# Kernel optimization log

Measured on AMD Instinct MI355X. Metric: run time of the kernel, lower is better.

Reference implementation:

```python
import jax, jax.numpy as jnp
import numpy as np

HEADS = 16
KV_HEADS = 4
HEAD_DIM = 64
EMBED = 1024


def setup_inputs() -> dict:
    key = jax.random.key(0)
    k1, k2, k3, k4, k5 = jax.random.split(key, 5)
    B, S, G, E = 1, 2048, 2, EMBED
    scale = 1.0 / np.sqrt(E)
    x = jax.random.normal(k1, (B, S, G, E), dtype=jnp.float32)
    Wq = jax.random.normal(k2, (E, HEADS * HEAD_DIM), dtype=jnp.float32) * scale
    Wk = jax.random.normal(k3, (E, KV_HEADS * HEAD_DIM), dtype=jnp.float32) * scale
    Wv = jax.random.normal(k4, (E, KV_HEADS * HEAD_DIM), dtype=jnp.float32) * scale
    Wo = jax.random.normal(k5, (E, E), dtype=jnp.float32) * scale
    return {"x": x, "Wq": Wq, "Wk": Wk, "Wv": Wv, "Wo": Wo}


def reference(x, Wq, Wk, Wv, Wo):
    B, S, G, E = x.shape
    ratio = HEADS // KV_HEADS
    # projections over last dim (no bias, no activation)
    q = (x @ Wq).reshape(B, S, G, HEADS, HEAD_DIM)
    k = (x @ Wk).reshape(B, S, G, KV_HEADS, HEAD_DIM)
    v = (x @ Wv).reshape(B, S, G, KV_HEADS, HEAD_DIM)
    # GQA repeat_kv: each kv head repeated `ratio` times consecutively
    k = jnp.repeat(k, ratio, axis=3)  # [B,S,G,H,D]
    v = jnp.repeat(v, ratio, axis=3)
    # energy: [B,G,H,Q,K]
    energy = jnp.einsum('bqghd,bkghd->bghqk', q, k)
    # causal mask: triu(1) set to -inf (before the sqrt scaling, as in source)
    causal = jnp.triu(jnp.ones((S, S), dtype=bool), 1)
    energy = jnp.where(causal, -jnp.inf, energy)
    scores = jax.nn.softmax(energy / np.sqrt(HEAD_DIM), axis=-1)
    attn = jnp.einsum('bghqv,bvghd->bqghd', scores, v)
    attn = attn.reshape(B, S, G, E)
    return attn @ Wo
```

## Files before the change

kernel.cpp:

```cpp
#include <hip/hip_runtime.h>
#include <cstdint>
#include <cstddef>

typedef __bf16 bf16_t;
typedef bf16_t bf16x8 __attribute__((ext_vector_type(8)));
typedef float f32x4 __attribute__((ext_vector_type(4)));

__device__ inline bf16x8 load8(const float* p) {
  f32x4 a = *reinterpret_cast<const f32x4*>(p);
  f32x4 b = *reinterpret_cast<const f32x4*>(p + 4);
  bf16x8 r;
  r[0] = (bf16_t)a[0]; r[1] = (bf16_t)a[1];
  r[2] = (bf16_t)a[2]; r[3] = (bf16_t)a[3];
  r[4] = (bf16_t)b[0]; r[5] = (bf16_t)b[1];
  r[6] = (bf16_t)b[2]; r[7] = (bf16_t)b[3];
  return r;
}
__device__ inline bf16x8 load8(const bf16_t* p) {
  return *reinterpret_cast<const bf16x8*>(p);
}

__device__ inline void gload_lds16(const bf16_t* g, bf16_t* l) {
  __builtin_amdgcn_global_load_lds(
      (const __attribute__((address_space(1))) void*)g,
      (__attribute__((address_space(3))) void*)l, 16, 0, 0);
}

__global__ __launch_bounds__(256) void cvt_all_k(
    const float* __restrict__ x, bf16_t* __restrict__ xb,
    const float* __restrict__ Wq, const float* __restrict__ Wk,
    const float* __restrict__ Wv, const float* __restrict__ Wo,
    bf16_t* __restrict__ wqT, bf16_t* __restrict__ wkT,
    bf16_t* __restrict__ wvT, bf16_t* __restrict__ woT) {
  __shared__ bf16_t Ts[64][72];
  const int tid = threadIdx.x;
  if (blockIdx.x < 2048) {
    const size_t i = (size_t)blockIdx.x * 2048 + (size_t)tid * 8;
    *reinterpret_cast<bf16x8*>(xb + i) = load8(x + i);
    return;
  }
  const int b = blockIdx.x - 2048;
  const float* S;
  bf16_t* D;
  int N, idx;
  if (b < 256) { S = Wq; D = wqT; N = 1024; idx = b; }
  else if (b < 320) { S = Wk; D = wkT; N = 256; idx = b - 256; }
  else if (b < 384) { S = Wv; D = wvT; N = 256; idx = b - 320; }
  else { S = Wo; D = woT; N = 1024; idx = b - 384; }
  const int ntl = (N == 1024) ? 4 : 2;
  const int kt0 = (idx >> ntl) * 64;
  const int n0 = (idx & ((1 << ntl) - 1)) * 64;
#pragma unroll
  for (int i = 0; i < 2; ++i) {
    const int c = tid + 256 * i;
    const int row = c >> 3, col0 = (c & 7) * 8;
    *reinterpret_cast<bf16x8*>(&Ts[row][col0]) =
        load8(&S[(size_t)(kt0 + row) * N + n0 + col0]);
  }
  __syncthreads();
#pragma unroll
  for (int i = 0; i < 2; ++i) {
    const int c = tid + 256 * i;
    const int nrow = c >> 3, k0 = (c & 7) * 8;
    bf16x8 v;
#pragma unroll
    for (int j = 0; j < 8; ++j) v[j] = Ts[k0 + j][nrow];
    *reinterpret_cast<bf16x8*>(&D[(size_t)(n0 + nrow) * 1024 + kt0 + k0]) = v;
  }
}

__device__ inline void stage_gldsA(const bf16_t* __restrict__ G, int grow0,
                                   int gK, int k0, bf16_t* lds, int w, int l) {
#pragma unroll
  for (int i = 0; i < 2; ++i) {
    const int seg = w * 2 + i;
    const int r = (seg << 4) + (l >> 2);
    const int cb = (l & 3) ^ ((r >> 1) & 3);
    gload_lds16(G + (size_t)(grow0 + r) * gK + k0 + cb * 8, lds + (seg << 9));
  }
}
__device__ inline void stage_gldsB(const bf16_t* __restrict__ G, int grow0,
                                   int gK, int k0, bf16_t* lds, int w, int l) {
  const int r = (w << 4) + (l >> 2);
  const int cb = (l & 3) ^ ((r >> 1) & 3);
  gload_lds16(G + (size_t)(grow0 + r) * gK + k0 + cb * 8, lds + (w << 9));
}

template <typename OutT>
__device__ inline void gemm_bt_body(const bf16_t* __restrict__ A,
                                    const bf16_t* __restrict__ BT,
                                    OutT* __restrict__ C, int m0, int bt0,
                                    int K, int CN, int cn0, float alpha) {
  __shared__ __align__(16) bf16_t As[2][128][32];
  __shared__ __align__(16) bf16_t Bs[2][64][32];

  const int tid = threadIdx.x;
  const int wave = tid >> 6, lane = tid & 63;
  const int quad = lane >> 4, l16 = lane & 15;
  const int moff = (wave & 1) * 64, noff = (wave >> 1) * 32;

  f32x4 acc[4][2];
#pragma unroll
  for (int mt = 0; mt < 4; ++mt)
#pragma unroll
    for (int nt = 0; nt < 2; ++nt) acc[mt][nt] = {0.f, 0.f, 0.f, 0.f};

  stage_gldsA(A, m0, K, 0, &As[0][0][0], wave, lane);
  stage_gldsB(BT, bt0, K, 0, &Bs[0][0][0], wave, lane);

  for (int k0 = 0; k0 < K; k0 += 32) {
    const int c = (k0 >> 5) & 1;
    __syncthreads();
    if (k0 + 32 < K) {
      stage_gldsA(A, m0, K, k0 + 32, &As[c ^ 1][0][0], wave, lane);
      stage_gldsB(BT, bt0, K, k0 + 32, &Bs[c ^ 1][0][0], wave, lane);
    }
    bf16x8 af[4], bfr[2];
#pragma unroll
    for (int mt = 0; mt < 4; ++mt) {
      const int row = moff + mt * 16 + l16;
      af[mt] = *reinterpret_cast<const bf16x8*>(
          &As[c][row][(quad ^ ((row >> 1) & 3)) * 8]);
    }
#pragma unroll
    for (int nt = 0; nt < 2; ++nt) {
      const int row = noff + nt * 16 + l16;
      bfr[nt] = *reinterpret_cast<const bf16x8*>(
          &Bs[c][row][(quad ^ ((row >> 1) & 3)) * 8]);
    }
#pragma unroll
    for (int mt = 0; mt < 4; ++mt)
#pragma unroll
      for (int nt = 0; nt < 2; ++nt)
        acc[mt][nt] = __builtin_amdgcn_mfma_f32_16x16x32_bf16(
            af[mt], bfr[nt], acc[mt][nt], 0, 0, 0);
  }

#pragma unroll
  for (int mt = 0; mt < 4; ++mt) {
    const int crow = m0 + moff + mt * 16 + quad * 4;
#pragma unroll
    for (int nt = 0; nt < 2; ++nt) {
      const int ccol = cn0 + noff + nt * 16 + l16;
#pragma unroll
      for (int r = 0; r < 4; ++r)
        C[(size_t)(crow + r) * CN + ccol] = (OutT)(acc[mt][nt][r] * alpha);
    }
  }
}

__global__ __launch_bounds__(256, 3) void qkv_k(
    const bf16_t* __restrict__ x, const bf16_t* __restrict__ wqT,
    const bf16_t* __restrict__ wkT, const bf16_t* __restrict__ wvT,
    bf16_t* __restrict__ Qo, bf16_t* __restrict__ Ko, bf16_t* __restrict__ Vo) {
  const int n0 = blockIdx.x * 64;
  const int m0 = blockIdx.y * 128;
  const bf16_t* BT;
  bf16_t* C;
  int CN, bn0;
  float alpha;
  if (n0 < 1024) {
    BT = wqT; C = Qo; CN = 1024; bn0 = n0; alpha = 0.125f;
  } else if (n0 < 1280) {
    BT = wkT; C = Ko; CN = 256; bn0 = n0 - 1024; alpha = 1.0f;
  } else {
    BT = wvT; C = Vo; CN = 256; bn0 = n0 - 1280; alpha = 1.0f;
  }
  gemm_bt_body<bf16_t>(x, BT, C, m0, bn0, 1024, CN, bn0, alpha);
}

template <typename OutT>
__global__ __launch_bounds__(256, 3) void gemm_bt_k(
    const bf16_t* __restrict__ A, const bf16_t* __restrict__ BT,
    OutT* __restrict__ C, int K, int N, float alpha) {
  gemm_bt_body<OutT>(A, BT, C, blockIdx.y * 128, blockIdx.x * 64, K, N,
                     blockIdx.x * 64, alpha);
}

__global__ __launch_bounds__(256) void transpose_v_k(
    const bf16_t* __restrict__ V, bf16_t* __restrict__ VT) {
  __shared__ bf16_t Vs[64][72];
  const int tid = threadIdx.x;
  const int kt0 = blockIdx.x * 64;
  const int ghk = blockIdx.y;
  const int g = ghk >> 2, kh = ghk & 3;
#pragma unroll
  for (int i = 0; i < 2; ++i) {
    const int c = tid + 256 * i;
    const int row = c >> 3, d0 = (c & 7) * 8;
    *reinterpret_cast<bf16x8*>(&Vs[row][d0]) = *reinterpret_cast<const bf16x8*>(
        &V[((size_t)(kt0 + row) * 2 + g) * 256 + kh * 64 + d0]);
  }
  __syncthreads();
#pragma unroll
  for (int i = 0; i < 2; ++i) {
    const int c = tid + 256 * i;
    const int d = c >> 3, k0 = (c & 7) * 8;
    bf16x8 v;
#pragma unroll
    for (int j = 0; j < 8; ++j) v[j] = Vs[k0 + j][d];
    *reinterpret_cast<bf16x8*>(&VT[((size_t)ghk * 64 + d) * 2048 + kt0 + k0]) =
        v;
  }
}

__global__ __launch_bounds__(256)
__attribute__((amdgpu_waves_per_eu(4, 4))) void flash11_k(
    const bf16_t* __restrict__ Q, const bf16_t* __restrict__ K,
    const bf16_t* __restrict__ VT, bf16_t* __restrict__ ATTN) {
  __shared__ __align__(16) bf16_t Ks[2][64][64];
  __shared__ __align__(16) bf16_t Vs[2][64][64];
  __shared__ __align__(16) bf16_t Ps[4][16][64];

  const int tid = threadIdx.x;
  const int w = tid >> 6, lane = tid & 63;
  const int quad = lane >> 4, l16 = lane & 15;
  const int b = blockIdx.x;
  const int gh = blockIdx.y;
  const int j8 = b & 7;
  const int i8e = ((b >> 3) + (gh >> 3)) & 3;
  const int T = (i8e == 0) ? j8
              : (i8e == 1) ? (15 - j8)
              : (i8e == 2) ? (16 + j8)
                           : (31 - j8);
  const int g = gh >> 4, h = gh & 15, kh = h >> 2;
  const int qrow0 = T * 64 + w * 16;
  const int swz = ((l16 >> 2) & 3) << 4;
  const int rsw = l16 & 7;

  bf16x8 qf[2];
#pragma unroll
  for (int t = 0; t < 2; ++t)
    qf[t] = *reinterpret_cast<const bf16x8*>(
        &Q[((size_t)(qrow0 + l16) * 2 + g) * 1024 + h * 64 + t * 32 +
           quad * 8]);

  f32x4 O[4];
  f32x4 lp = {0.f, 0.f, 0.f, 0.f};
#pragma unroll
  for (int d = 0; d < 4; ++d) O[d] = {0.f, 0.f, 0.f, 0.f};

  bf16x8 kr[2], vr[2];
  auto load_tile = [&](int nt0) {
#pragma unroll
    for (int i = 0; i < 2; ++i) {
      const int c = tid + 256 * i;
      const int row = c >> 3, e0 = (c & 7) * 8;
      kr[i] = *reinterpret_cast<const bf16x8*>(
          &K[((size_t)(nt0 + row) * 2 + g) * 256 + kh * 64 + e0]);
      vr[i] = *reinterpret_cast<const bf16x8*>(
          &VT[((size_t)(g * 4 + kh) * 64 + row) * 2048 + nt0 + e0]);
    }
  };
  auto stage_tile = [&](int buf) {
#pragma unroll
    for (int i = 0; i < 2; ++i) {
      const int c = tid + 256 * i;
      const int row = c >> 3;
      const int pb = (((c & 7) ^ (row & 7)) << 3);
      *reinterpret_cast<bf16x8*>(&Ks[buf][row][pb]) = kr[i];
      *reinterpret_cast<bf16x8*>(&Vs[buf][row][pb]) = vr[i];
    }
  };

  load_tile(0);
  stage_tile(0);
  if (T > 0) load_tile(64);
  __syncthreads();

  int cbuf = 0;
  for (int kt = 0; kt <= T; ++kt) {
    if (kt < T) stage_tile(cbuf ^ 1);
    if (kt + 2 <= T) load_tile((kt + 2) * 64);

    f32x4 s[4];
    __builtin_amdgcn_s_setprio(1);
#pragma unroll
    for (int nt = 0; nt < 4; ++nt) {
      bf16x8 kf0 = *reinterpret_cast<const bf16x8*>(
          &Ks[cbuf][nt * 16 + l16][(quad ^ rsw) << 3]);
      bf16x8 kf1 = *reinterpret_cast<const bf16x8*>(
          &Ks[cbuf][nt * 16 + l16][((4 + quad) ^ rsw) << 3]);
      f32x4 z = {0.f, 0.f, 0.f, 0.f};
      z = __builtin_amdgcn_mfma_f32_16x16x32_bf16(qf[0], kf0, z, 0, 0, 0);
      s[nt] = __builtin_amdgcn_mfma_f32_16x16x32_bf16(qf[1], kf1, z, 0, 0, 0);
    }
    __builtin_amdgcn_s_setprio(0);
    const bool diag = (kt == T);
    const int qloc = w * 16 + quad * 4;
#pragma unroll
    for (int nt = 0; nt < 4; ++nt) {
      const int key = nt * 16 + l16;
#pragma unroll
      for (int r = 0; r < 4; ++r) {
        float p = __expf(s[nt][r]);
        if (diag && key > qloc + r) p = 0.f;
        lp[r] += p;
        Ps[w][quad * 4 + r][((nt ^ quad) << 4) + l16] = (bf16_t)p;
      }
    }
    bf16x8 pf[2];
#pragma unroll
    for (int t = 0; t < 2; ++t)
      pf[t] = *reinterpret_cast<const bf16x8*>(
          &Ps[w][l16][(t * 32 + quad * 8) ^ swz]);
    __builtin_amdgcn_s_setprio(1);
#pragma unroll
    for (int dnt = 0; dnt < 4; ++dnt) {
      bf16x8 vf0 = *reinterpret_cast<const bf16x8*>(
          &Vs[cbuf][dnt * 16 + l16][(quad ^ rsw) << 3]);
      bf16x8 vf1 = *reinterpret_cast<const bf16x8*>(
          &Vs[cbuf][dnt * 16 + l16][((4 + quad) ^ rsw) << 3]);
      O[dnt] = __builtin_amdgcn_mfma_f32_16x16x32_bf16(pf[0], vf0, O[dnt], 0,
                                                       0, 0);
      O[dnt] = __builtin_amdgcn_mfma_f32_16x16x32_bf16(pf[1], vf1, O[dnt], 0,
                                                       0, 0);
    }
    __builtin_amdgcn_s_setprio(0);
    __syncthreads();
    cbuf ^= 1;
  }

#pragma unroll
  for (int off = 1; off < 16; off <<= 1)
#pragma unroll
    for (int r = 0; r < 4; ++r) lp[r] += __shfl_xor(lp[r], off, 64);
#pragma unroll
  for (int r = 0; r < 4; ++r) {
    const float inv = 1.f / lp[r];
    const int row = qrow0 + quad * 4 + r;
#pragma unroll
    for (int dnt = 0; dnt < 4; ++dnt)
      ATTN[((size_t)row * 2 + g) * 1024 + h * 64 + dnt * 16 + l16] =
          (bf16_t)(O[dnt][r] * inv);
  }
}

extern "C" void kernel_launch(void* const* d_in, const int* in_sizes, int n_in,
                              void* d_out, int out_size, void* d_ws,
                              size_t ws_size, hipStream_t stream) {
  (void)in_sizes;
  (void)n_in;
  (void)out_size;
  (void)ws_size;

  const float* x = (const float*)d_in[0];
  const float* Wq = (const float*)d_in[1];
  const float* Wk = (const float*)d_in[2];
  const float* Wv = (const float*)d_in[3];
  const float* Wo = (const float*)d_in[4];
  float* out = (float*)d_out;

  const size_t MB = 1024 * 1024;
  char* ob = (char*)d_out;
  bf16_t* Qtmp = (bf16_t*)ob;
  bf16_t* VTws = (bf16_t*)(ob + 8 * MB);
  bf16_t* wqT = (bf16_t*)(ob + 10 * MB);
  bf16_t* wkT = (bf16_t*)(ob + 12 * MB);
  bf16_t* wvT = (bf16_t*)(ob + 12 * MB + 512 * 1024);
  bf16_t* Vws = (bf16_t*)(ob + 13 * MB);
  char* wb = (char*)d_ws;
  bf16_t* Kws = (bf16_t*)wb;
  bf16_t* woT = (bf16_t*)(wb + 2 * MB);
  bf16_t* ATTNws = (bf16_t*)(wb + 4 * MB);
  bf16_t* xb = ATTNws;

  cvt_all_k<<<dim3(2688), dim3(256), 0, stream>>>(x, xb, Wq, Wk, Wv, Wo, wqT,
                                                  wkT, wvT, woT);
  qkv_k<<<dim3(24, 32), dim3(256), 0, stream>>>(xb, wqT, wkT, wvT, Qtmp, Kws,
                                                Vws);
  transpose_v_k<<<dim3(32, 8), dim3(256), 0, stream>>>(Vws, VTws);
  flash11_k<<<dim3(32, 32), dim3(256), 0, stream>>>(Qtmp, Kws, VTws, ATTNws);
  gemm_bt_k<float><<<dim3(16, 32), dim3(256), 0, stream>>>(ATTNws, woT, out,
                                                           1024, 1024, 1.0f);
}
```

Measured before the change: 168.1 us.

## Use two waves per flash block, each handling 32 query rows

The flash attention kernel now runs 128 threads (2 waves) per block instead of 4 waves, and each wave processes two 16-row query groups. K/V fragments read from LDS are reused across both row groups, which halves LDS fragment reads per MFMA. Each thread loads twice as much of each tile. The cost is higher register pressure (doubled accumulators, scores and Q fragments) and fewer waves to hide latency per block.

Measured after the change: 173.8 us. +3.4%, slower.

```diff
diff --git a/kernel.cpp b/kernel.cpp
--- a/kernel.cpp
+++ b/kernel.cpp
@@ -204,13 +204,12 @@
   }
 }
 
-__global__ __launch_bounds__(256)
-__attribute__((amdgpu_waves_per_eu(4, 4))) void flash11_k(
+__global__ __launch_bounds__(128, 2) void flash12_k(
     const bf16_t* __restrict__ Q, const bf16_t* __restrict__ K,
     const bf16_t* __restrict__ VT, bf16_t* __restrict__ ATTN) {
   __shared__ __align__(16) bf16_t Ks[2][64][64];
   __shared__ __align__(16) bf16_t Vs[2][64][64];
-  __shared__ __align__(16) bf16_t Ps[4][16][64];
+  __shared__ __align__(16) bf16_t Ps[2][32][64];
 
   const int tid = threadIdx.x;
   const int w = tid >> 6, lane = tid & 63;
@@ -224,27 +223,33 @@
               : (i8e == 2) ? (16 + j8)
                            : (31 - j8);
   const int g = gh >> 4, h = gh & 15, kh = h >> 2;
-  const int qrow0 = T * 64 + w * 16;
+  const int qbase = T * 64 + w * 32;
   const int swz = ((l16 >> 2) & 3) << 4;
   const int rsw = l16 & 7;
 
-  bf16x8 qf[2];
-#pragma unroll
-  for (int t = 0; t < 2; ++t)
-    qf[t] = *reinterpret_cast<const bf16x8*>(
-        &Q[((size_t)(qrow0 + l16) * 2 + g) * 1024 + h * 64 + t * 32 +
-           quad * 8]);
-
-  f32x4 O[4];
-  f32x4 lp = {0.f, 0.f, 0.f, 0.f};
-#pragma unroll
-  for (int d = 0; d < 4; ++d) O[d] = {0.f, 0.f, 0.f, 0.f};
-
-  bf16x8 kr[2], vr[2];
+  bf16x8 qf[2][2];
+#pragma unroll
+  for (int rg = 0; rg < 2; ++rg)
+#pragma unroll
+    for (int t = 0; t < 2; ++t)
+      qf[rg][t] = *reinterpret_cast<const bf16x8*>(
+          &Q[((size_t)(qbase + rg * 16 + l16) * 2 + g) * 1024 + h * 64 +
+             t * 32 + quad * 8]);
+
+  f32x4 O[2][4];
+  f32x4 lp[2];
+#pragma unroll
+  for (int rg = 0; rg < 2; ++rg) {
+    lp[rg] = {0.f, 0.f, 0.f, 0.f};
+#pragma unroll
+    for (int d = 0; d < 4; ++d) O[rg][d] = {0.f, 0.f, 0.f, 0.f};
+  }
+
+  bf16x8 kr[4], vr[4];
   auto load_tile = [&](int nt0) {
 #pragma unroll
-    for (int i = 0; i < 2; ++i) {
-      const int c = tid + 256 * i;
+    for (int i = 0; i < 4; ++i) {
+      const int c = tid + 128 * i;
       const int row = c >> 3, e0 = (c & 7) * 8;
       kr[i] = *reinterpret_cast<const bf16x8*>(
           &K[((size_t)(nt0 + row) * 2 + g) * 256 + kh * 64 + e0]);
@@ -254,8 +259,8 @@
   };
   auto stage_tile = [&](int buf) {
 #pragma unroll
-    for (int i = 0; i < 2; ++i) {
-      const int c = tid + 256 * i;
+    for (int i = 0; i < 4; ++i) {
+      const int c = tid + 128 * i;
       const int row = c >> 3;
       const int pb = (((c & 7) ^ (row & 7)) << 3);
       *reinterpret_cast<bf16x8*>(&Ks[buf][row][pb]) = kr[i];
@@ -273,7 +278,7 @@
     if (kt < T) stage_tile(cbuf ^ 1);
     if (kt + 2 <= T) load_tile((kt + 2) * 64);
 
-    f32x4 s[4];
+    f32x4 s[2][4];
     __builtin_amdgcn_s_setprio(1);
 #pragma unroll
     for (int nt = 0; nt < 4; ++nt) {
@@ -281,29 +286,37 @@
           &Ks[cbuf][nt * 16 + l16][(quad ^ rsw) << 3]);
       bf16x8 kf1 = *reinterpret_cast<const bf16x8*>(
           &Ks[cbuf][nt * 16 + l16][((4 + quad) ^ rsw) << 3]);
-      f32x4 z = {0.f, 0.f, 0.f, 0.f};
-      z = __builtin_amdgcn_mfma_f32_16x16x32_bf16(qf[0], kf0, z, 0, 0, 0);
-      s[nt] = __builtin_amdgcn_mfma_f32_16x16x32_bf16(qf[1], kf1, z, 0, 0, 0);
+#pragma unroll
+      for (int rg = 0; rg < 2; ++rg) {
+        f32x4 z = {0.f, 0.f, 0.f, 0.f};
+        z = __builtin_amdgcn_mfma_f32_16x16x32_bf16(qf[rg][0], kf0, z, 0, 0, 0);
+        s[rg][nt] =
+            __builtin_amdgcn_mfma_f32_16x16x32_bf16(qf[rg][1], kf1, z, 0, 0, 0);
+      }
     }
     __builtin_amdgcn_s_setprio(0);
     const bool diag = (kt == T);
-    const int qloc = w * 16 + quad * 4;
-#pragma unroll
-    for (int nt = 0; nt < 4; ++nt) {
-      const int key = nt * 16 + l16;
-#pragma unroll
-      for (int r = 0; r < 4; ++r) {
-        float p = __expf(s[nt][r]);
-        if (diag && key > qloc + r) p = 0.f;
-        lp[r] += p;
-        Ps[w][quad * 4 + r][((nt ^ quad) << 4) + l16] = (bf16_t)p;
+#pragma unroll
+    for (int rg = 0; rg < 2; ++rg) {
+#pragma unroll
+      for (int nt = 0; nt < 4; ++nt) {
+        const int key = nt * 16 + l16;
+#pragma unroll
+        for (int r = 0; r < 4; ++r) {
+          float p = __expf(s[rg][nt][r]);
+          if (diag && key > w * 32 + rg * 16 + quad * 4 + r) p = 0.f;
+          lp[rg][r] += p;
+          Ps[w][rg * 16 + quad * 4 + r][((nt ^ quad) << 4) + l16] = (bf16_t)p;
+        }
       }
     }
-    bf16x8 pf[2];
-#pragma unroll
-    for (int t = 0; t < 2; ++t)
-      pf[t] = *reinterpret_cast<const bf16x8*>(
-          &Ps[w][l16][(t * 32 + quad * 8) ^ swz]);
+    bf16x8 pf[2][2];
+#pragma unroll
+    for (int rg = 0; rg < 2; ++rg)
+#pragma unroll
+      for (int t = 0; t < 2; ++t)
+        pf[rg][t] = *reinterpret_cast<const bf16x8*>(
+            &Ps[w][rg * 16 + l16][(t * 32 + quad * 8) ^ swz]);
     __builtin_amdgcn_s_setprio(1);
 #pragma unroll
     for (int dnt = 0; dnt < 4; ++dnt) {
@@ -311,10 +324,13 @@
           &Vs[cbuf][dnt * 16 + l16][(quad ^ rsw) << 3]);
       bf16x8 vf1 = *reinterpret_cast<const bf16x8*>(
           &Vs[cbuf][dnt * 16 + l16][((4 + quad) ^ rsw) << 3]);
-      O[dnt] = __builtin_amdgcn_mfma_f32_16x16x32_bf16(pf[0], vf0, O[dnt], 0,
-                                                       0, 0);
-      O[dnt] = __builtin_amdgcn_mfma_f32_16x16x32_bf16(pf[1], vf1, O[dnt], 0,
-                                                       0, 0);
+#pragma unroll
+      for (int rg = 0; rg < 2; ++rg) {
+        O[rg][dnt] = __builtin_amdgcn_mfma_f32_16x16x32_bf16(
+            pf[rg][0], vf0, O[rg][dnt], 0, 0, 0);
+        O[rg][dnt] = __builtin_amdgcn_mfma_f32_16x16x32_bf16(
+            pf[rg][1], vf1, O[rg][dnt], 0, 0, 0);
+      }
     }
     __builtin_amdgcn_s_setprio(0);
     __syncthreads();
@@ -322,17 +338,20 @@
   }
 
 #pragma unroll
-  for (int off = 1; off < 16; off <<= 1)
-#pragma unroll
-    for (int r = 0; r < 4; ++r) lp[r] += __shfl_xor(lp[r], off, 64);
-#pragma unroll
-  for (int r = 0; r < 4; ++r) {
-    const float inv = 1.f / lp[r];
-    const int row = qrow0 + quad * 4 + r;
-#pragma unroll
-    for (int dnt = 0; dnt < 4; ++dnt)
-      ATTN[((size_t)row * 2 + g) * 1024 + h * 64 + dnt * 16 + l16] =
-          (bf16_t)(O[dnt][r] * inv);
+  for (int rg = 0; rg < 2; ++rg) {
+#pragma unroll
+    for (int off = 1; off < 16; off <<= 1)
+#pragma unroll
+      for (int r = 0; r < 4; ++r) lp[rg][r] += __shfl_xor(lp[rg][r], off, 64);
+#pragma unroll
+    for (int r = 0; r < 4; ++r) {
+      const float inv = 1.f / lp[rg][r];
+      const int row = qbase + rg * 16 + quad * 4 + r;
+#pragma unroll
+      for (int dnt = 0; dnt < 4; ++dnt)
+        ATTN[((size_t)row * 2 + g) * 1024 + h * 64 + dnt * 16 + l16] =
+            (bf16_t)(O[rg][dnt][r] * inv);
+    }
   }
 }
 
@@ -370,7 +389,7 @@
   qkv_k<<<dim3(24, 32), dim3(256), 0, stream>>>(xb, wqT, wkT, wvT, Qtmp, Kws,
                                                 Vws);
   transpose_v_k<<<dim3(32, 8), dim3(256), 0, stream>>>(Vws, VTws);
-  flash11_k<<<dim3(32, 32), dim3(256), 0, stream>>>(Qtmp, Kws, VTws, ATTNws);
+  flash12_k<<<dim3(32, 32), dim3(128), 0, stream>>>(Qtmp, Kws, VTws, ATTNws);
   gemm_bt_k<float><<<dim3(16, 32), dim3(256), 0, stream>>>(ATTNws, woT, out,
                                                            1024, 1024, 1.0f);
 }
```
